# Kernel optimization log

Measured on AMD Instinct MI355X. Metric: run time of the kernel, lower is better.

Reference implementation:

```python
import jax, jax.numpy as jnp
import numpy as np

B, S, D_IN, D_OUT = 4, 2048, 4096, 4096
ACT_BITS = 8
GROUP_SIZE = 64
EPS = 1e-5


def _ste(x, q):
    # straight-through estimator: forward value q, gradient of identity
    return x + jax.lax.stop_gradient(q - x)


def absmax_quantize_dequant(x, bits=ACT_BITS, group_size=GROUP_SIZE):
    # per-token, per-group absmax fake quantization along the last dim
    qmax = float(2 ** (bits - 1) - 1)  # 127 for 8 bits
    *lead, d = x.shape
    g = group_size if group_size is not None else d
    xg = x.reshape(*lead, d // g, g)
    absmax = jnp.max(jnp.abs(xg), axis=-1, keepdims=True)
    scale = qmax / jnp.clip(absmax, EPS, None)
    q = jnp.clip(jnp.round(xg * scale), -qmax, qmax) / scale
    q = q.reshape(*lead, d)
    return _ste(x, q)


def ternary_weight_quantize_absmean(w, per_row=True):
    # BitNet b1.58: scale = mean(|W|) per output row; W_t in {-s, 0, s}
    axis = (1,) if per_row else (0, 1)
    s = jnp.mean(jnp.abs(w), axis=axis, keepdims=True)
    s = jnp.clip(s, EPS, None)
    q = jnp.clip(jnp.round(w / s), -1.0, 1.0) * s
    return _ste(w, q)


def setup_inputs() -> dict:
    key = jax.random.key(0)
    k1, k2 = jax.random.split(key)
    x = jax.random.normal(k1, (B, S, D_IN), dtype=jnp.float32)
    # kaiming-uniform-ish init scale
    bound = float(np.sqrt(1.0 / D_IN))
    weight = jax.random.uniform(k2, (D_OUT, D_IN), dtype=jnp.float32,
                                minval=-bound, maxval=bound)
    return {"x": x, "weight": weight}


def reference(x, weight):
    x_q = absmax_quantize_dequant(x)                      # [B,S,D_in]
    w_t = ternary_weight_quantize_absmean(weight)         # [D_out,D_in]
    return jnp.einsum("bsi,oi->bso", x_q, w_t)            # [B,S,D_out]
```

## Files before the change

### kernel.cpp

```cpp
#include <hip/hip_runtime.h>
#include <stdint.h>

constexpr int M = 4 * 2048;
constexpr int K = 4096;
constexpr int N = 4096;
constexpr float EPSf = 1e-5f;
constexpr float QMAX = 127.0f;

typedef __attribute__((ext_vector_type(8))) short bf16x8;
typedef __attribute__((ext_vector_type(4))) float f32x4;
typedef __attribute__((ext_vector_type(8))) unsigned short ushort8;

__device__ __forceinline__ unsigned short f2bf(float f) {
  union { float f; uint32_t u; } c; c.f = f;
  uint32_t u = c.u;
  return (unsigned short)((u + 0x7fffu + ((u >> 16) & 1u)) >> 16);
}

__device__ __forceinline__ void async_copy16(const void* g, const void* l) {
  __builtin_amdgcn_global_load_lds(
      (const __attribute__((address_space(1))) unsigned int*)g,
      (__attribute__((address_space(3))) unsigned int*)l, 16, 0, 0);
}

__global__ void __launch_bounds__(256) quant_fused_kernel(
    const float* __restrict__ x, unsigned short* __restrict__ xq,
    const float* __restrict__ w, unsigned short* __restrict__ wt,
    float* __restrict__ wscale) {
  const int tid = threadIdx.x;
  if (blockIdx.x < 4096) {
    const int row = blockIdx.x;
    const float* wr = w + (long)row * K;
    float4 v[4];
    float s = 0.f;
    #pragma unroll
    for (int p = 0; p < 4; p++) {
      v[p] = ((const float4*)wr)[tid + p * 256];
      s += fabsf(v[p].x) + fabsf(v[p].y) + fabsf(v[p].z) + fabsf(v[p].w);
    }
    #pragma unroll
    for (int d = 1; d < 64; d <<= 1) s += __shfl_xor(s, d);
    __shared__ float red[4];
    if ((tid & 63) == 0) red[tid >> 6] = s;
    __syncthreads();
    const float tot = red[0] + red[1] + red[2] + red[3];
    const float sc = fmaxf(tot / (float)K, EPSf);
    if (tid == 0) wscale[row] = sc;
    unsigned short* wrow = wt + (long)row * K;
    #pragma unroll
    for (int p = 0; p < 4; p++) {
      ushort4 o;
      o.x = f2bf(fminf(fmaxf(rintf(v[p].x / sc), -1.f), 1.f));
      o.y = f2bf(fminf(fmaxf(rintf(v[p].y / sc), -1.f), 1.f));
      o.z = f2bf(fminf(fmaxf(rintf(v[p].z / sc), -1.f), 1.f));
      o.w = f2bf(fminf(fmaxf(rintf(v[p].w / sc), -1.f), 1.f));
      ((ushort4*)wrow)[tid + p * 256] = o;
    }
  } else {
    const int t = ((int)blockIdx.x - 4096) * 256 + tid;
    const float4 v0 = ((const float4*)x)[2 * t];
    const float4 v1 = ((const float4*)x)[2 * t + 1];
    float m = fmaxf(
        fmaxf(fmaxf(fabsf(v0.x), fabsf(v0.y)), fmaxf(fabsf(v0.z), fabsf(v0.w))),
        fmaxf(fmaxf(fabsf(v1.x), fabsf(v1.y)), fmaxf(fabsf(v1.z), fabsf(v1.w))));
    #pragma unroll
    for (int d = 1; d < 8; d <<= 1) m = fmaxf(m, __shfl_xor(m, d));
    m = fmaxf(m, EPSf);
    const float scale = QMAX / m;
    const float invs  = m * (1.0f / QMAX);
    const float q[8] = {v0.x, v0.y, v0.z, v0.w, v1.x, v1.y, v1.z, v1.w};
    ushort8 o;
    #pragma unroll
    for (int e = 0; e < 8; e++) {
      const float r = fminf(fmaxf(rintf(q[e] * scale), -QMAX), QMAX);
      o[e] = f2bf(r * invs);
    }
    ((ushort8*)xq)[t] = o;
  }
}


#define BAR() do { asm volatile("" ::: "memory"); \
                   __builtin_amdgcn_s_barrier();  \
                   asm volatile("" ::: "memory"); } while (0)
#define LGKM0() asm volatile("s_waitcnt lgkmcnt(0)" ::: "memory")
#define VMCNT(n) asm volatile("s_waitcnt vmcnt(" #n ")" ::: "memory")

__global__ void __launch_bounds__(512, 2) gemm_bt_kernel(const short* __restrict__ A,
                                                         const short* __restrict__ Bt,
                                                         const float* __restrict__ wscale,
                                                         float* __restrict__ C) {
  __shared__ short smem[65536];

  const int tid  = (int)threadIdx.x;
  const int lane = tid & 63;
  const int wv   = tid >> 6;
  const int wm = wv & 1, wn = wv >> 1;
  const int quad = lane >> 4, r16 = lane & 15;

  const int f = (int)blockIdx.x;
  const int s = (f & 7) * 64 + (f >> 3);
  const int m0 = (s >> 4) * 256;
  const int n0 = (s & 15) * 256;

  const short* Ab = A  + (long)m0 * K;
  const short* Bb = Bt + (long)n0 * K;

  const int s_row8 = tid >> 3;
  const int s_kc   = ((tid & 7) ^ (s_row8 & 7)) * 8;

  const int ksw0 = (((quad * 16)      ) ^ ((r16 & 7) << 4)) >> 1;
  const int ksw1 = (((quad * 16) + 64 ) ^ ((r16 & 7) << 4)) >> 1;
  const int aro  = (wm * 64 + r16) * 64;
  const int bro  = (wn * 32 + r16) * 64;

  f32x4 acc[8][4];
  #pragma unroll
  for (int i = 0; i < 8; i++)
    #pragma unroll
    for (int j = 0; j < 4; j++) acc[i][j] = (f32x4){0.f, 0.f, 0.f, 0.f};

  bf16x8 af[4][2];
  bf16x8 bf_[2][2][2];

#define STAGE_A(buf, hh, kt) do {                                              \
    short* _d = smem + (buf) * 32768 + (hh) * 8192 + tid * 8;                  \
    const short* _g = Ab + (long)((hh) * 64 + s_row8) * K + (kt) * 64 + s_kc;  \
    async_copy16(_g, _d);                                                      \
    async_copy16(_g + (long)128 * K, _d + 4096);                               \
  } while (0)

#define STAGE_B(buf, hh, kt) do {                                              \
    short* _d = smem + (buf) * 32768 + 16384 + (hh) * 8192 + tid * 8;          \
    const int _r0 = (tid >> 8) * 64 + (hh) * 32 + (s_row8 & 31);               \
    const short* _g = Bb + (long)_r0 * K + (kt) * 64 + s_kc;                   \
    async_copy16(_g, _d);                                                      \
    async_copy16(_g + (long)128 * K, _d + 4096);                               \
  } while (0)

#define LOAD_A(buf, mi) do {                                                   \
    const short* _b = smem + (buf) * 32768 + (mi) * 8192 + aro;                \
    _Pragma("unroll") for (int _mt = 0; _mt < 4; ++_mt) {                      \
      af[_mt][0] = *(const bf16x8*)(_b + _mt * 1024 + ksw0);                   \
      af[_mt][1] = *(const bf16x8*)(_b + _mt * 1024 + ksw1);                   \
    }                                                                          \
  } while (0)

#define LOAD_B(buf, nj) do {                                                   \
    const short* _b = smem + (buf) * 32768 + 16384 + (nj) * 8192 + bro;        \
    _Pragma("unroll") for (int _nt = 0; _nt < 2; ++_nt) {                      \
      bf_[nj][_nt][0] = *(const bf16x8*)(_b + _nt * 1024 + ksw0);              \
      bf_[nj][_nt][1] = *(const bf16x8*)(_b + _nt * 1024 + ksw1);              \
    }                                                                          \
  } while (0)

#define MFMA_PHASE(mi, nj) do {                                                \
    BAR(); LGKM0();                                                            \
    __builtin_amdgcn_s_setprio(1);                                             \
    _Pragma("unroll") for (int _mt = 0; _mt < 4; ++_mt)                        \
    _Pragma("unroll") for (int _nt = 0; _nt < 2; ++_nt) {                      \
      acc[(mi)*4+_mt][(nj)*2+_nt] = __builtin_amdgcn_mfma_f32_16x16x32_bf16(   \
          af[_mt][0], bf_[nj][_nt][0], acc[(mi)*4+_mt][(nj)*2+_nt], 0, 0, 0);  \
      acc[(mi)*4+_mt][(nj)*2+_nt] = __builtin_amdgcn_mfma_f32_16x16x32_bf16(   \
          af[_mt][1], bf_[nj][_nt][1], acc[(mi)*4+_mt][(nj)*2+_nt], 0, 0, 0);  \
    }                                                                          \
    __builtin_amdgcn_s_setprio(0);                                             \
  } while (0)

  STAGE_A(0, 0, 0); STAGE_B(0, 0, 0); STAGE_B(0, 1, 0); STAGE_A(0, 1, 0);
  VMCNT(4);
  STAGE_A(1, 0, 1); STAGE_B(1, 0, 1); STAGE_B(1, 1, 1);
  VMCNT(6);
  BAR();

  for (int kt = 0; kt < 64; kt += 2) {
    const bool g2 = (kt + 2) < 64;
    const bool g3 = (kt + 3) < 64;

    LOAD_A(0, 0); LOAD_B(0, 0);
    STAGE_A(1, 1, kt + 1);
    MFMA_PHASE(0, 0); BAR();
    LOAD_B(0, 1);
    if (g2) STAGE_A(0, 0, kt + 2);
    MFMA_PHASE(0, 1); BAR();
    LOAD_A(0, 1);
    if (g2) STAGE_B(0, 0, kt + 2);
    MFMA_PHASE(1, 1); BAR();
    if (g2) STAGE_B(0, 1, kt + 2);
    MFMA_PHASE(1, 0);
    if (kt == 62) { VMCNT(0); } else { VMCNT(6); }
    BAR();

    LOAD_A(1, 0); LOAD_B(1, 0);
    if (g2) STAGE_A(0, 1, kt + 2);
    MFMA_PHASE(0, 0); BAR();
    LOAD_B(1, 1);
    if (g3) STAGE_A(1, 0, kt + 3);
    MFMA_PHASE(0, 1); BAR();
    LOAD_A(1, 1);
    if (g3) STAGE_B(1, 0, kt + 3);
    MFMA_PHASE(1, 1); BAR();
    if (g3) STAGE_B(1, 1, kt + 3);
    MFMA_PHASE(1, 0);
    if (g2) { VMCNT(6); BAR(); }
  }

  #pragma unroll
  for (int an = 0; an < 4; ++an) {
    const int col = n0 + wn * 64 + (an >> 1) * 32 + (an & 1) * 16 + r16;
    const float sc = wscale[col];
    #pragma unroll
    for (int am = 0; am < 8; ++am) {
      const int rb = m0 + wm * 128 + (am >> 2) * 64 + (am & 3) * 16 + quad * 4;
      #pragma unroll
      for (int r = 0; r < 4; ++r)
        C[(long)(rb + r) * N + col] = acc[am][an][r] * sc;
    }
  }
}

extern "C" void kernel_launch(void* const* d_in, const int* in_sizes, int n_in,
                              void* d_out, int out_size, void* d_ws, size_t ws_size,
                              hipStream_t stream) {
  const float* x   = (const float*)d_in[0];
  const float* wgt = (const float*)d_in[1];
  float* out = (float*)d_out;

  unsigned short* Aq = (unsigned short*)d_ws;
  unsigned short* Tq = Aq + (size_t)M * K;
  float* wscale = (float*)(Tq + (size_t)N * K);

  quant_fused_kernel<<<4096 + (M * K / 8) / 256, 256, 0, stream>>>(
      x, Aq, wgt, Tq, wscale);

  gemm_bt_kernel<<<dim3(512), dim3(512), 0, stream>>>((const short*)Aq, (const short*)Tq,
                                                      wscale, out);
}
```

Before: 477.1 us.

## Switch GEMM inner loop to 32x32x16 bf16 MFMA tiles

Replaces the 16x16x32 bf16 MFMA instructions with 32x32x16 MFMAs. Each wave's 128x64 subtile is now covered by 4x2 32x32 accumulators instead of 8x4 16x16 ones, and the LDS fragment loads and epilogue row mapping are reworked to match the new lane layout. Larger MFMA tiles issue fewer instructions and fewer LDS fragment reads per FLOP. The change also adds an extra lgkmcnt(8) wait before the first MFMA phase, which may shift how LDS reads overlap with the async copies.

```diff
diff --git a/kernel.cpp b/kernel.cpp
--- a/kernel.cpp
+++ b/kernel.cpp
@@ -8,7 +8,7 @@
 constexpr float QMAX = 127.0f;
 
 typedef __attribute__((ext_vector_type(8))) short bf16x8;
-typedef __attribute__((ext_vector_type(4))) float f32x4;
+typedef __attribute__((ext_vector_type(16))) float f32x16;
 typedef __attribute__((ext_vector_type(8))) unsigned short ushort8;
 
 __device__ __forceinline__ unsigned short f2bf(float f) {
@@ -84,6 +84,7 @@
                    __builtin_amdgcn_s_barrier();  \
                    asm volatile("" ::: "memory"); } while (0)
 #define LGKM0() asm volatile("s_waitcnt lgkmcnt(0)" ::: "memory")
+#define LGKM8() asm volatile("s_waitcnt lgkmcnt(8)" ::: "memory")
 #define VMCNT(n) asm volatile("s_waitcnt vmcnt(" #n ")" ::: "memory")
 
 __global__ void __launch_bounds__(512, 2) gemm_bt_kernel(const short* __restrict__ A,
@@ -96,7 +97,9 @@
   const int lane = tid & 63;
   const int wv   = tid >> 6;
   const int wm = wv & 1, wn = wv >> 1;
-  const int quad = lane >> 4, r16 = lane & 15;
+  const int hi  = lane >> 5;
+  const int l31 = lane & 31;
+  const int l7  = lane & 7;
 
   const int f = (int)blockIdx.x;
   const int s = (f & 7) * 64 + (f >> 3);
@@ -109,19 +112,23 @@
   const int s_row8 = tid >> 3;
   const int s_kc   = ((tid & 7) ^ (s_row8 & 7)) * 8;
 
-  const int ksw0 = (((quad * 16)      ) ^ ((r16 & 7) << 4)) >> 1;
-  const int ksw1 = (((quad * 16) + 64 ) ^ ((r16 & 7) << 4)) >> 1;
-  const int aro  = (wm * 64 + r16) * 64;
-  const int bro  = (wn * 32 + r16) * 64;
-
-  f32x4 acc[8][4];
+  int ksw[4];
   #pragma unroll
-  for (int i = 0; i < 8; i++)
-    #pragma unroll
-    for (int j = 0; j < 4; j++) acc[i][j] = (f32x4){0.f, 0.f, 0.f, 0.f};
-
-  bf16x8 af[4][2];
-  bf16x8 bf_[2][2][2];
+  for (int kq = 0; kq < 4; ++kq)
+    ksw[kq] = ((((kq * 2 + hi) * 16) ^ (l7 << 4)) >> 1);
+  const int aroA = (wm * 64 + l31) * 64;
+  const int broB = (wn * 32 + l31) * 64;
+
+  f32x16 acc[4][2];
+  #pragma unroll
+  for (int i = 0; i < 4; i++)
+    #pragma unroll
+    for (int j = 0; j < 2; j++)
+      #pragma unroll
+      for (int r = 0; r < 16; r++) acc[i][j][r] = 0.f;
+
+  bf16x8 af[2][4];
+  bf16x8 bf_[2][4];
 
 #define STAGE_A(buf, hh, kt) do {                                              \
     short* _d = smem + (buf) * 32768 + (hh) * 8192 + tid * 8;                  \
@@ -139,30 +146,25 @@
   } while (0)
 
 #define LOAD_A(buf, mi) do {                                                   \
-    const short* _b = smem + (buf) * 32768 + (mi) * 8192 + aro;                \
-    _Pragma("unroll") for (int _mt = 0; _mt < 4; ++_mt) {                      \
-      af[_mt][0] = *(const bf16x8*)(_b + _mt * 1024 + ksw0);                   \
-      af[_mt][1] = *(const bf16x8*)(_b + _mt * 1024 + ksw1);                   \
-    }                                                                          \
-  } while (0)
-
-#define LOAD_B(buf, nj) do {                                                   \
-    const short* _b = smem + (buf) * 32768 + 16384 + (nj) * 8192 + bro;        \
-    _Pragma("unroll") for (int _nt = 0; _nt < 2; ++_nt) {                      \
-      bf_[nj][_nt][0] = *(const bf16x8*)(_b + _nt * 1024 + ksw0);              \
-      bf_[nj][_nt][1] = *(const bf16x8*)(_b + _nt * 1024 + ksw1);              \
-    }                                                                          \
-  } while (0)
-
-#define MFMA_PHASE(mi, nj) do {                                                \
+    const short* _b = smem + (buf) * 32768 + (mi) * 8192 + aroA;               \
+    _Pragma("unroll") for (int _a2 = 0; _a2 < 2; ++_a2)                        \
+    _Pragma("unroll") for (int _kq = 0; _kq < 4; ++_kq)                        \
+      af[_a2][_kq] = *(const bf16x8*)(_b + _a2 * 2048 + ksw[_kq]);             \
+  } while (0)
+
+#define LOAD_B(buf, ng) do {                                                   \
+    const short* _b = smem + (buf) * 32768 + 16384 + (ng) * 8192 + broB;       \
+    _Pragma("unroll") for (int _kq = 0; _kq < 4; ++_kq)                        \
+      bf_[ng][_kq] = *(const bf16x8*)(_b + ksw[_kq]);                          \
+  } while (0)
+
+#define MFMA_PHASE(mi, ng) do {                                                \
     BAR(); LGKM0();                                                            \
     __builtin_amdgcn_s_setprio(1);                                             \
-    _Pragma("unroll") for (int _mt = 0; _mt < 4; ++_mt)                        \
-    _Pragma("unroll") for (int _nt = 0; _nt < 2; ++_nt) {                      \
-      acc[(mi)*4+_mt][(nj)*2+_nt] = __builtin_amdgcn_mfma_f32_16x16x32_bf16(   \
-          af[_mt][0], bf_[nj][_nt][0], acc[(mi)*4+_mt][(nj)*2+_nt], 0, 0, 0);  \
-      acc[(mi)*4+_mt][(nj)*2+_nt] = __builtin_amdgcn_mfma_f32_16x16x32_bf16(   \
-          af[_mt][1], bf_[nj][_nt][1], acc[(mi)*4+_mt][(nj)*2+_nt], 0, 0, 0);  \
+    _Pragma("unroll") for (int _kq = 0; _kq < 4; ++_kq)                        \
+    _Pragma("unroll") for (int _a2 = 0; _a2 < 2; ++_a2) {                      \
+      acc[(mi)*2+_a2][ng] = __builtin_amdgcn_mfma_f32_32x32x16_bf16(           \
+          af[_a2][_kq], bf_[ng][_kq], acc[(mi)*2+_a2][ng], 0, 0, 0);           \
     }                                                                          \
     __builtin_amdgcn_s_setprio(0);                                             \
   } while (0)
@@ -179,6 +181,7 @@
 
     LOAD_A(0, 0); LOAD_B(0, 0);
     STAGE_A(1, 1, kt + 1);
+    LGKM8();
     MFMA_PHASE(0, 0); BAR();
     LOAD_B(0, 1);
     if (g2) STAGE_A(0, 0, kt + 2);
@@ -193,6 +196,7 @@
 
     LOAD_A(1, 0); LOAD_B(1, 0);
     if (g2) STAGE_A(0, 1, kt + 2);
+    LGKM8();
     MFMA_PHASE(0, 0); BAR();
     LOAD_B(1, 1);
     if (g3) STAGE_A(1, 0, kt + 3);
@@ -206,15 +210,17 @@
   }
 
   #pragma unroll
-  for (int an = 0; an < 4; ++an) {
-    const int col = n0 + wn * 64 + (an >> 1) * 32 + (an & 1) * 16 + r16;
+  for (int ng = 0; ng < 2; ++ng) {
+    const int col = n0 + wn * 64 + ng * 32 + l31;
     const float sc = wscale[col];
     #pragma unroll
-    for (int am = 0; am < 8; ++am) {
-      const int rb = m0 + wm * 128 + (am >> 2) * 64 + (am & 3) * 16 + quad * 4;
+    for (int am = 0; am < 4; ++am) {
+      const int rbase = m0 + wm * 128 + am * 32 + 4 * hi;
       #pragma unroll
-      for (int r = 0; r < 4; ++r)
-        C[(long)(rb + r) * N + col] = acc[am][an][r] * sc;
+      for (int reg = 0; reg < 16; ++reg) {
+        const int row = rbase + (reg & 3) + 8 * (reg >> 2);
+        C[(long)row * N + col] = acc[am][ng][reg] * sc;
+      }
     }
   }
 }
```

Result: slower. 495.2 us (+3.8%).

## Switch GEMM to single LDS buffer with intra-tile staged prefetch

Applied to the files above, without the earlier changes.

Halves shared memory from 128KB to 64KB by dropping the double buffer. Each quarter of the next k-tile is staged into the slot as soon as the current tile's reads from that slot finish. The smaller LDS footprint could let two 512-thread blocks fit per CU, as the launch bounds request. The cost is less prefetch distance, so global loads get less time to hide behind MFMA work, and the vmcnt and barrier ordering must be exactly right to avoid overwriting data that is still being read.

```diff
diff --git a/kernel.cpp b/kernel.cpp
--- a/kernel.cpp
+++ b/kernel.cpp
@@ -90,7 +90,7 @@
                                                          const short* __restrict__ Bt,
                                                          const float* __restrict__ wscale,
                                                          float* __restrict__ C) {
-  __shared__ short smem[65536];
+  __shared__ short smem[32768];
 
   const int tid  = (int)threadIdx.x;
   const int lane = tid & 63;
@@ -123,31 +123,31 @@
   bf16x8 af[4][2];
   bf16x8 bf_[2][2][2];
 
-#define STAGE_A(buf, hh, kt) do {                                              \
-    short* _d = smem + (buf) * 32768 + (hh) * 8192 + tid * 8;                  \
+#define STAGE_A(hh, kt) do {                                                   \
+    short* _d = smem + (hh) * 8192 + tid * 8;                                  \
     const short* _g = Ab + (long)((hh) * 64 + s_row8) * K + (kt) * 64 + s_kc;  \
     async_copy16(_g, _d);                                                      \
     async_copy16(_g + (long)128 * K, _d + 4096);                               \
   } while (0)
 
-#define STAGE_B(buf, hh, kt) do {                                              \
-    short* _d = smem + (buf) * 32768 + 16384 + (hh) * 8192 + tid * 8;          \
+#define STAGE_B(hh, kt) do {                                                   \
+    short* _d = smem + 16384 + (hh) * 8192 + tid * 8;                          \
     const int _r0 = (tid >> 8) * 64 + (hh) * 32 + (s_row8 & 31);               \
     const short* _g = Bb + (long)_r0 * K + (kt) * 64 + s_kc;                   \
     async_copy16(_g, _d);                                                      \
     async_copy16(_g + (long)128 * K, _d + 4096);                               \
   } while (0)
 
-#define LOAD_A(buf, mi) do {                                                   \
-    const short* _b = smem + (buf) * 32768 + (mi) * 8192 + aro;                \
+#define LOAD_A(mi) do {                                                        \
+    const short* _b = smem + (mi) * 8192 + aro;                                \
     _Pragma("unroll") for (int _mt = 0; _mt < 4; ++_mt) {                      \
       af[_mt][0] = *(const bf16x8*)(_b + _mt * 1024 + ksw0);                   \
       af[_mt][1] = *(const bf16x8*)(_b + _mt * 1024 + ksw1);                   \
     }                                                                          \
   } while (0)
 
-#define LOAD_B(buf, nj) do {                                                   \
-    const short* _b = smem + (buf) * 32768 + 16384 + (nj) * 8192 + bro;        \
+#define LOAD_B(nj) do {                                                        \
+    const short* _b = smem + 16384 + (nj) * 8192 + bro;                        \
     _Pragma("unroll") for (int _nt = 0; _nt < 2; ++_nt) {                      \
       bf_[nj][_nt][0] = *(const bf16x8*)(_b + _nt * 1024 + ksw0);              \
       bf_[nj][_nt][1] = *(const bf16x8*)(_b + _nt * 1024 + ksw1);              \
@@ -167,42 +167,31 @@
     __builtin_amdgcn_s_setprio(0);                                             \
   } while (0)
 
-  STAGE_A(0, 0, 0); STAGE_B(0, 0, 0); STAGE_B(0, 1, 0); STAGE_A(0, 1, 0);
+  STAGE_A(0, 0); STAGE_B(0, 0); STAGE_B(1, 0); STAGE_A(1, 0);
   VMCNT(4);
-  STAGE_A(1, 0, 1); STAGE_B(1, 0, 1); STAGE_B(1, 1, 1);
-  VMCNT(6);
   BAR();
 
-  for (int kt = 0; kt < 64; kt += 2) {
-    const bool g2 = (kt + 2) < 64;
-    const bool g3 = (kt + 3) < 64;
-
-    LOAD_A(0, 0); LOAD_B(0, 0);
-    STAGE_A(1, 1, kt + 1);
-    MFMA_PHASE(0, 0); BAR();
-    LOAD_B(0, 1);
-    if (g2) STAGE_A(0, 0, kt + 2);
-    MFMA_PHASE(0, 1); BAR();
-    LOAD_A(0, 1);
-    if (g2) STAGE_B(0, 0, kt + 2);
-    MFMA_PHASE(1, 1); BAR();
-    if (g2) STAGE_B(0, 1, kt + 2);
+  for (int kt = 0; kt < 64; ++kt) {
+    const bool g = kt < 63;
+    LOAD_A(0); LOAD_B(0);
+    MFMA_PHASE(0, 0);
+    VMCNT(2);
+    BAR();
+    LOAD_B(1);
+    if (g) { STAGE_A(0, kt + 1); STAGE_B(0, kt + 1); }
+    MFMA_PHASE(0, 1);
+    if (g) { VMCNT(4); } else { VMCNT(0); }
+    BAR();
+    LOAD_A(1);
+    if (g) STAGE_B(1, kt + 1);
+    MFMA_PHASE(1, 1);
+    BAR();
+    if (g) STAGE_A(1, kt + 1);
     MFMA_PHASE(1, 0);
-    if (kt == 62) { VMCNT(0); } else { VMCNT(6); }
-    BAR();
-
-    LOAD_A(1, 0); LOAD_B(1, 0);
-    if (g2) STAGE_A(0, 1, kt + 2);
-    MFMA_PHASE(0, 0); BAR();
-    LOAD_B(1, 1);
-    if (g3) STAGE_A(1, 0, kt + 3);
-    MFMA_PHASE(0, 1); BAR();
-    LOAD_A(1, 1);
-    if (g3) STAGE_B(1, 0, kt + 3);
-    MFMA_PHASE(1, 1); BAR();
-    if (g3) STAGE_B(1, 1, kt + 3);
-    MFMA_PHASE(1, 0);
-    if (g2) { VMCNT(6); BAR(); }
+    if (g) {
+      VMCNT(4);
+      BAR();
+    }
   }
 
   #pragma unroll
```

After: 473.4 us. About the same (-0.8%).
